# Kernel optimization log

Hardware: AMD Instinct MI355X
Metric: run time of the kernel (lower is better)

## Reference

```python
import jax, jax.numpy as jnp
import numpy as np

HIDDEN = 1024
HEADS = 16
HEAD_DIM = HIDDEN // HEADS


def setup_inputs() -> dict:
    key = jax.random.key(0)
    ks = jax.random.split(key, 5)
    x = jax.random.normal(ks[0], (4, 2048, HIDDEN), dtype=jnp.float32)
    s = 1.0 / np.sqrt(HIDDEN)
    W_qkv = jax.random.normal(ks[1], (HIDDEN, 3 * HIDDEN), dtype=jnp.float32) * s
    b_qkv = jax.random.normal(ks[2], (3 * HIDDEN,), dtype=jnp.float32) * s
    W_out = jax.random.normal(ks[3], (HIDDEN, HIDDEN), dtype=jnp.float32) * s
    b_out = jax.random.normal(ks[4], (HIDDEN,), dtype=jnp.float32) * s
    return {"x": x, "W_qkv": W_qkv, "b_qkv": b_qkv, "W_out": W_out, "b_out": b_out}


def reference(x, W_qkv, b_qkv, W_out, b_out):
    B, S, _ = x.shape
    qkv = x @ W_qkv + b_qkv                       # [B,S,3H]
    qkv = qkv.reshape(B, S, 3, HEADS, HEAD_DIM)
    q, k, v = jnp.moveaxis(qkv, 2, 0)             # each [B,S,nh,hd]
    scale = 1.0 / np.sqrt(HEAD_DIM)
    scores = jnp.einsum('bqhd,bkhd->bhqk', q, k) * scale
    probs = jax.nn.softmax(scores, axis=-1)       # dropout p=0 (eval): identity
    attn = jnp.einsum('bhqk,bkhd->bqhd', probs, v)
    attn = attn.reshape(B, S, HIDDEN)
    return attn @ W_out + b_out
```

## Files before the change

### kernel.cpp

```cpp
#include <hip/hip_runtime.h>

#define SEQ    2048
#define BATCH  4
#define HID    1024
#define NH     16
#define MTOT   (BATCH * SEQ)

typedef __attribute__((ext_vector_type(8)))  short          short8;
typedef __attribute__((ext_vector_type(4)))  float          f32x4;
typedef __attribute__((ext_vector_type(16))) float          f32x16;
typedef __attribute__((ext_vector_type(8)))  unsigned short ushort8v;

#define QSCL 0.1803368801111204f

__device__ __forceinline__ float bf2f(unsigned short u) {
    return __uint_as_float(((unsigned int)u) << 16);
}
__device__ __forceinline__ unsigned short f2bf(float f) {
    unsigned int u = __float_as_uint(f);
    u += 0x7fffu + ((u >> 16) & 1u);
    return (unsigned short)(u >> 16);
}
__device__ __forceinline__ unsigned int pk2bf(float lo, float hi) {
    unsigned int ul = __float_as_uint(lo) + 0x8000u;
    unsigned int uh = __float_as_uint(hi) + 0x8000u;
    return __builtin_amdgcn_perm(uh, ul, 0x07060302u);
}

__device__ __forceinline__ void gl_lds16(const void* g, void* l) {
    __builtin_amdgcn_global_load_lds(
        (__attribute__((address_space(1))) void*)g,
        (__attribute__((address_space(3))) void*)l, 16, 0, 0);
}

__device__ __forceinline__ int swz64(int row, int col) {
    return row * 64 + ((((col >> 3) ^ (row & 7))) << 3) + (col & 7);
}

__device__ __forceinline__ int gidx_of(int row, int kq) {
    return (row * 4 + ((kq + (row >> 1)) & 3)) * 8;
}

__global__ __launch_bounds__(256)
void cvt_x(const float* __restrict__ x, unsigned short* __restrict__ xb)
{
    const size_t i = ((size_t)blockIdx.x * 256 + threadIdx.x) * 4;
    const float4 f = *(const float4*)(x + i);
    uint2 u;
    u.x = pk2bf(f.x, f.y);
    u.y = pk2bf(f.z, f.w);
    *(uint2*)(xb + i) = u;
}

__global__ __launch_bounds__(256)
void transpose_cvt(const float* __restrict__ W, unsigned short* __restrict__ Wt,
                   int K, int N)
{
    __shared__ unsigned short T[32][33];
    const int n0 = blockIdx.x * 32, k0 = blockIdx.y * 32;
    const int tr = threadIdx.x >> 3, tc = (threadIdx.x & 7) * 4;
    const float4 f = *(const float4*)(W + (size_t)(k0 + tr) * N + n0 + tc);
    T[tr][tc + 0] = f2bf(f.x);
    T[tr][tc + 1] = f2bf(f.y);
    T[tr][tc + 2] = f2bf(f.z);
    T[tr][tc + 3] = f2bf(f.w);
    __syncthreads();
    ushort4 u;
    u.x = T[tc + 0][tr]; u.y = T[tc + 1][tr];
    u.z = T[tc + 2][tr]; u.w = T[tc + 3][tr];
    *(ushort4*)(Wt + (size_t)(n0 + tr) * K + k0 + tc) = u;
}

template<bool OUTF32, bool VSPLIT>
__global__ __launch_bounds__(256)
void gemm_mfma(const unsigned short* __restrict__ A,
               const unsigned short* __restrict__ Bt,
               const float* __restrict__ bias, void* __restrict__ Cptr,
               unsigned short* __restrict__ Vt,
               int lda, int ldc, int K)
{
    __shared__ unsigned short As[128 * 32];
    __shared__ unsigned short Bs[128 * 32];

    const int tid = threadIdx.x;
    const int wave = tid >> 6, lane = tid & 63;
    const int quad = lane >> 4, lm = lane & 15;
    const int wm = wave & 1, wn = wave >> 1;
    const int m0 = blockIdx.y * 128, n0 = blockIdx.x * 128;

    const unsigned short* aSrc[2];
    const unsigned short* bSrc[2];
    unsigned short* aDst[2];
    unsigned short* bDst[2];
    #pragma unroll
    for (int j = 0; j < 2; ++j) {
        const int g = (wave * 2 + j) * 64 + lane;
        const int row = g >> 2;
        const int kq = ((g & 3) - (row >> 1)) & 3;
        aSrc[j] = A  + (size_t)(m0 + row) * lda + kq * 8;
        bSrc[j] = Bt + (size_t)(n0 + row) * K   + kq * 8;
        aDst[j] = &As[g * 8];
        bDst[j] = &Bs[g * 8];
    }

    f32x4 acc[4][4];
    #pragma unroll
    for (int i = 0; i < 4; ++i)
        #pragma unroll
        for (int j = 0; j < 4; ++j)
            acc[i][j] = (f32x4){0.f, 0.f, 0.f, 0.f};

    int aOff[4], bOff[4];
    #pragma unroll
    for (int i = 0; i < 4; ++i) {
        aOff[i] = gidx_of(wm * 64 + i * 16 + lm, quad);
        bOff[i] = gidx_of(wn * 64 + i * 16 + lm, quad);
    }

    for (int k0 = 0; k0 < K; k0 += 32) {
        __syncthreads();
        gl_lds16(aSrc[0] + k0, aDst[0]);
        gl_lds16(aSrc[1] + k0, aDst[1]);
        gl_lds16(bSrc[0] + k0, bDst[0]);
        gl_lds16(bSrc[1] + k0, bDst[1]);
        __syncthreads();

        short8 af[4], bf[4];
        #pragma unroll
        for (int i = 0; i < 4; ++i) af[i] = *(const short8*)&As[aOff[i]];
        #pragma unroll
        for (int j = 0; j < 4; ++j) bf[j] = *(const short8*)&Bs[bOff[j]];
        #pragma unroll
        for (int i = 0; i < 4; ++i)
            #pragma unroll
            for (int j = 0; j < 4; ++j)
                acc[i][j] = __builtin_amdgcn_mfma_f32_16x16x32_bf16(
                    af[i], bf[j], acc[i][j], 0, 0, 0);
    }

    float bj[4];
    #pragma unroll
    for (int j = 0; j < 4; ++j) bj[j] = bias[n0 + wn * 64 + j * 16 + lm];

    #pragma unroll
    for (int i = 0; i < 4; ++i) {
        #pragma unroll
        for (int j = 0; j < 4; ++j) {
            const int col = n0 + wn * 64 + j * 16 + lm;
            #pragma unroll
            for (int rr = 0; rr < 4; ++rr) {
                const int row = m0 + wm * 64 + i * 16 + quad * 4 + rr;
                float v = acc[i][j][rr] + bj[j];
                if (VSPLIT) {
                    if (col >= 2048) {
                        const int dg = col - 2048;
                        const int b = row >> 11, s = row & 2047;
                        Vt[((size_t)b * 1024 + dg) * 2048 + s] = f2bf(v);
                    } else {
                        if (col < 1024) v *= QSCL;
                        ((unsigned short*)Cptr)[(size_t)row * ldc + col] = f2bf(v);
                    }
                } else if (OUTF32) {
                    ((float*)Cptr)[(size_t)row * ldc + col] = v;
                } else {
                    ((unsigned short*)Cptr)[(size_t)row * ldc + col] = f2bf(v);
                }
            }
        }
    }
}

__global__ __launch_bounds__(256, 2)
void attn_mfma(unsigned short* __restrict__ qk,
               const unsigned short* __restrict__ Vt)
{
    const int qt = blockIdx.x, hh = blockIdx.y, b = blockIdx.z;
    const size_t row0 = (size_t)b * SEQ;
    const int tid = threadIdx.x;
    const int wave = tid >> 6, lane = tid & 63;
    const int l5 = lane >> 5, lm = lane & 31;

    __shared__ unsigned short Ks[64 * 64];
    __shared__ unsigned short Vst[64 * 64];
    __shared__ unsigned short Ps[4][64 * 64];

    const int qbase = qt * 256 + wave * 64;

    short8 qf[2][4];
    #pragma unroll
    for (int qg = 0; qg < 2; ++qg)
        #pragma unroll
        for (int ks = 0; ks < 4; ++ks)
            qf[qg][ks] = *(const short8*)(
                qk + (row0 + qbase + qg * 32 + lm) * 2048 + hh * 64 + ks * 16 + l5 * 8);

    f32x16 oacc[2][2];
    #pragma unroll
    for (int dg = 0; dg < 2; ++dg)
        #pragma unroll
        for (int qg = 0; qg < 2; ++qg)
            #pragma unroll
            for (int e = 0; e < 16; ++e) oacc[dg][qg][e] = 0.f;
    float lrun[2] = {0.f, 0.f};

    const int srow = tid >> 2;
    const int scol = (tid & 3) * 16;

    const unsigned short* kbase = qk + 1024 + hh * 64;
    const unsigned short* vbase = Vt + ((size_t)b * 1024 + hh * 64 + srow) * 2048;

    ushort8v kp0, kp1, vp0, vp1;
    {
        const unsigned short* kp = kbase + (row0 + srow) * 2048 + scol;
        kp0 = *(const ushort8v*)kp;  kp1 = *(const ushort8v*)(kp + 8);
        vp0 = *(const ushort8v*)(vbase + scol);
        vp1 = *(const ushort8v*)(vbase + scol + 8);
    }

    for (int kt = 0; kt < SEQ; kt += 64) {
        __syncthreads();
        *(ushort8v*)&Ks[swz64(srow, scol)]      = kp0;
        *(ushort8v*)&Ks[swz64(srow, scol + 8)]  = kp1;
        *(ushort8v*)&Vst[swz64(srow, scol)]     = vp0;
        *(ushort8v*)&Vst[swz64(srow, scol + 8)] = vp1;
        __syncthreads();

        {
            const int nk = (kt + 64 < SEQ) ? kt + 64 : kt;
            const unsigned short* kp = kbase + (row0 + nk + srow) * 2048 + scol;
            kp0 = *(const ushort8v*)kp;  kp1 = *(const ushort8v*)(kp + 8);
            vp0 = *(const ushort8v*)(vbase + nk + scol);
            vp1 = *(const ushort8v*)(vbase + nk + scol + 8);
        }

        #pragma unroll
        for (int kg = 0; kg < 2; ++kg) {
            f32x16 s[2];
            #pragma unroll
            for (int qg = 0; qg < 2; ++qg)
                #pragma unroll
                for (int e = 0; e < 16; ++e) s[qg][e] = 0.f;
            #pragma unroll
            for (int ks = 0; ks < 4; ++ks) {
                const short8 aK =
                    *(const short8*)&Ks[swz64(kg * 32 + lm, ks * 16 + l5 * 8)];
                #pragma unroll
                for (int qg = 0; qg < 2; ++qg)
                    s[qg] = __builtin_amdgcn_mfma_f32_32x32x16_bf16(
                        aK, qf[qg][ks], s[qg], 0, 0, 0);
            }
            #pragma unroll
            for (int qg = 0; qg < 2; ++qg) {
                float ls = 0.f;
                #pragma unroll
                for (int rg = 0; rg < 4; ++rg) {
                    const float p0 = exp2f(s[qg][rg * 4 + 0]);
                    const float p1 = exp2f(s[qg][rg * 4 + 1]);
                    const float p2 = exp2f(s[qg][rg * 4 + 2]);
                    const float p3 = exp2f(s[qg][rg * 4 + 3]);
                    ls += (p0 + p1) + (p2 + p3);
                    uint2 pk;
                    pk.x = pk2bf(p0, p1);
                    pk.y = pk2bf(p2, p3);
                    *(uint2*)&Ps[wave][swz64(qg * 32 + lm,
                                             kg * 32 + rg * 8 + l5 * 4)] = pk;
                }
                lrun[qg] += ls;
            }
        }

        #pragma unroll
        for (int ks = 0; ks < 4; ++ks) {
            const short8 aV0 = *(const short8*)&Vst[swz64(lm,      ks * 16 + l5 * 8)];
            const short8 aV1 = *(const short8*)&Vst[swz64(32 + lm, ks * 16 + l5 * 8)];
            #pragma unroll
            for (int qg = 0; qg < 2; ++qg) {
                const short8 bP =
                    *(const short8*)&Ps[wave][swz64(qg * 32 + lm, ks * 16 + l5 * 8)];
                oacc[0][qg] = __builtin_amdgcn_mfma_f32_32x32x16_bf16(
                    aV0, bP, oacc[0][qg], 0, 0, 0);
                oacc[1][qg] = __builtin_amdgcn_mfma_f32_32x32x16_bf16(
                    aV1, bP, oacc[1][qg], 0, 0, 0);
            }
        }
    }

    float linv[2];
    #pragma unroll
    for (int qg = 0; qg < 2; ++qg) {
        const float lt = lrun[qg] + __shfl_xor(lrun[qg], 32);
        linv[qg] = 1.f / lt;
    }

    #pragma unroll
    for (int dg = 0; dg < 2; ++dg)
        #pragma unroll
        for (int qg = 0; qg < 2; ++qg) {
            unsigned short* orow =
                qk + (row0 + qbase + qg * 32 + lm) * 2048 + hh * 64;
            #pragma unroll
            for (int rg = 0; rg < 4; ++rg) {
                const int d0 = dg * 32 + rg * 8 + l5 * 4;
                ushort4 st;
                st.x = f2bf(oacc[dg][qg][rg * 4 + 0] * linv[qg]);
                st.y = f2bf(oacc[dg][qg][rg * 4 + 1] * linv[qg]);
                st.z = f2bf(oacc[dg][qg][rg * 4 + 2] * linv[qg]);
                st.w = f2bf(oacc[dg][qg][rg * 4 + 3] * linv[qg]);
                *(ushort4*)(orow + d0) = st;
            }
        }
}

__global__ __launch_bounds__(256)
void qproj(const float* __restrict__ A, const float* __restrict__ W,
           const float* __restrict__ bias, unsigned short* __restrict__ outus)
{
    __shared__ float As[64][17];
    __shared__ float Bs[16][64];
    const int tid = threadIdx.x;
    const int tx = tid & 15, ty = tid >> 4;
    const int m0 = blockIdx.y * 64, n0 = blockIdx.x * 64;
    const int ar = tid >> 2, ac = (tid & 3) * 4;
    const int br = tid >> 4, bc = (tid & 15) * 4;
    float acc[4][4] = {{0.f}};
    for (int k0 = 0; k0 < HID; k0 += 16) {
        const float4 av = *(const float4*)(A + (size_t)(m0 + ar) * HID + k0 + ac);
        As[ar][ac + 0] = av.x; As[ar][ac + 1] = av.y;
        As[ar][ac + 2] = av.z; As[ar][ac + 3] = av.w;
        *(float4*)&Bs[br][bc] =
            *(const float4*)(W + (size_t)(k0 + br) * 3072 + n0 + bc);
        __syncthreads();
        #pragma unroll
        for (int kk = 0; kk < 16; ++kk) {
            float a[4];
            #pragma unroll
            for (int i = 0; i < 4; ++i) a[i] = As[ty * 4 + i][kk];
            const float4 b4 = *(const float4*)&Bs[kk][tx * 4];
            const float bv[4] = {b4.x, b4.y, b4.z, b4.w};
            #pragma unroll
            for (int i = 0; i < 4; ++i)
                #pragma unroll
                for (int j = 0; j < 4; ++j)
                    acc[i][j] = fmaf(a[i], bv[j], acc[i][j]);
        }
        __syncthreads();
    }
    float bb[4];
    #pragma unroll
    for (int j = 0; j < 4; ++j) bb[j] = bias[n0 + tx * 4 + j];
    #pragma unroll
    for (int i = 0; i < 4; ++i) {
        ushort4 st;
        st.x = f2bf(acc[i][0] + bb[0]); st.y = f2bf(acc[i][1] + bb[1]);
        st.z = f2bf(acc[i][2] + bb[2]); st.w = f2bf(acc[i][3] + bb[3]);
        *(ushort4*)(outus + (size_t)(m0 + ty * 4 + i) * 2048 + 1024 + n0 + tx * 4) = st;
    }
}

__global__ __launch_bounds__(256)
void kv_inplace(const float* __restrict__ W, const float* __restrict__ bias,
                unsigned short* __restrict__ xu)
{
    const float* xf = (const float*)xu;
    __shared__ unsigned short Asb[16][1032];
    __shared__ float Bs[16][68];
    const int tid = threadIdx.x;
    const int m0 = blockIdx.x * 16;
    const int tx = tid & 15, ty = tid >> 4;
    #pragma unroll 4
    for (int i = 0; i < 16; ++i) {
        const float4 v = *(const float4*)(xf + (size_t)(m0 + i) * HID + tid * 4);
        ushort4 s;
        s.x = f2bf(v.x); s.y = f2bf(v.y); s.z = f2bf(v.z); s.w = f2bf(v.w);
        *(ushort4*)&Asb[i][tid * 4] = s;
    }
    __syncthreads();
    for (int n0 = 0; n0 < 2048; n0 += 64) {
        float acc[4] = {0.f, 0.f, 0.f, 0.f};
        for (int k0 = 0; k0 < HID; k0 += 16) {
            *(float4*)&Bs[ty][tx * 4] =
                *(const float4*)(W + (size_t)(k0 + ty) * 3072 + 1024 + n0 + tx * 4);
            __syncthreads();
            #pragma unroll
            for (int kk = 0; kk < 16; ++kk) {
                const float a = bf2f(Asb[ty][k0 + kk]);
                const float4 b4 = *(const float4*)&Bs[kk][tx * 4];
                acc[0] = fmaf(a, b4.x, acc[0]); acc[1] = fmaf(a, b4.y, acc[1]);
                acc[2] = fmaf(a, b4.z, acc[2]); acc[3] = fmaf(a, b4.w, acc[3]);
            }
            __syncthreads();
        }
        const int n = n0 + tx * 4;
        ushort4 s;
        s.x = f2bf(acc[0] + bias[1024 + n + 0]);
        s.y = f2bf(acc[1] + bias[1024 + n + 1]);
        s.z = f2bf(acc[2] + bias[1024 + n + 2]);
        s.w = f2bf(acc[3] + bias[1024 + n + 3]);
        *(ushort4*)(xu + (size_t)(m0 + ty) * 2048 + n) = s;
    }
}

__global__ __launch_bounds__(256)
void attn_fwd(const unsigned short* __restrict__ xu,
              unsigned short* __restrict__ outus)
{
    const int qt = blockIdx.x, h = blockIdx.y, b = blockIdx.z;
    const int s0 = qt * 16;
    const size_t row0 = (size_t)b * SEQ;
    const int tid = threadIdx.x;
    const int qi = tid >> 4, tj = tid & 15;
    __shared__ float Ksh[64][68];
    __shared__ float Vsh[64][68];
    __shared__ float Psh[16][68];
    float qreg[64];
    {
        const uint4* qp =
            (const uint4*)(outus + (row0 + s0 + qi) * 2048 + 1024 + h * 64);
        #pragma unroll
        for (int i = 0; i < 8; ++i) {
            uint4 u = qp[i];
            const unsigned int w[4] = {u.x, u.y, u.z, u.w};
            #pragma unroll
            for (int j = 0; j < 4; ++j) {
                qreg[i * 8 + j * 2 + 0] = __uint_as_float(w[j] << 16) * 0.125f;
                qreg[i * 8 + j * 2 + 1] = __uint_as_float(w[j] & 0xffff0000u) * 0.125f;
            }
        }
    }
    float mrun = -1e30f, lrunv = 0.f;
    float oacc[4] = {0.f, 0.f, 0.f, 0.f};
    const int lr = tid >> 3, lc = (tid & 7) * 8;
    for (int kt = 0; kt < SEQ; kt += 64) {
        __syncthreads();
        #pragma unroll
        for (int half = 0; half < 2; ++half) {
            const int r = lr + half * 32;
            const size_t rowoff = (row0 + kt + r) * 2048 + h * 64 + lc;
            uint4 ku = *(const uint4*)(xu + rowoff);
            uint4 vu = *(const uint4*)(xu + rowoff + 1024);
            float4 f0, f1;
            f0.x = __uint_as_float(ku.x << 16); f0.y = __uint_as_float(ku.x & 0xffff0000u);
            f0.z = __uint_as_float(ku.y << 16); f0.w = __uint_as_float(ku.y & 0xffff0000u);
            f1.x = __uint_as_float(ku.z << 16); f1.y = __uint_as_float(ku.z & 0xffff0000u);
            f1.z = __uint_as_float(ku.w << 16); f1.w = __uint_as_float(ku.w & 0xffff0000u);
            *(float4*)&Ksh[r][lc]     = f0;
            *(float4*)&Ksh[r][lc + 4] = f1;
            f0.x = __uint_as_float(vu.x << 16); f0.y = __uint_as_float(vu.x & 0xffff0000u);
            f0.z = __uint_as_float(vu.y << 16); f0.w = __uint_as_float(vu.y & 0xffff0000u);
            f1.x = __uint_as_float(vu.z << 16); f1.y = __uint_as_float(vu.z & 0xffff0000u);
            f1.z = __uint_as_float(vu.w << 16); f1.w = __uint_as_float(vu.w & 0xffff0000u);
            *(float4*)&Vsh[r][lc]     = f0;
            *(float4*)&Vsh[r][lc + 4] = f1;
        }
        __syncthreads();
        float sc[4];
        #pragma unroll
        for (int u = 0; u < 4; ++u) {
            const int kk = tj + 16 * u;
            float s = 0.f;
            #pragma unroll
            for (int d = 0; d < 64; ++d) s = fmaf(qreg[d], Ksh[kk][d], s);
            sc[u] = s;
        }
        float tmax = fmaxf(fmaxf(sc[0], sc[1]), fmaxf(sc[2], sc[3]));
        #pragma unroll
        for (int off = 8; off >= 1; off >>= 1)
            tmax = fmaxf(tmax, __shfl_xor(tmax, off, 16));
        const float mnew = fmaxf(mrun, tmax);
        const float alpha = __expf(mrun - mnew);
        float psum = 0.f;
        #pragma unroll
        for (int u = 0; u < 4; ++u) {
            const float p = __expf(sc[u] - mnew);
            Psh[qi][tj + 16 * u] = p;
            psum += p;
        }
        #pragma unroll
        for (int off = 8; off >= 1; off >>= 1)
            psum += __shfl_xor(psum, off, 16);
        lrunv = lrunv * alpha + psum;
        mrun = mnew;
        oacc[0] *= alpha; oacc[1] *= alpha; oacc[2] *= alpha; oacc[3] *= alpha;
        __syncthreads();
        #pragma unroll 8
        for (int kk = 0; kk < 64; ++kk) {
            const float p = Psh[qi][kk];
            const float4 v4 = *(const float4*)&Vsh[kk][tj * 4];
            oacc[0] = fmaf(p, v4.x, oacc[0]); oacc[1] = fmaf(p, v4.y, oacc[1]);
            oacc[2] = fmaf(p, v4.z, oacc[2]); oacc[3] = fmaf(p, v4.w, oacc[3]);
        }
    }
    const float inv = 1.f / lrunv;
    ushort4 st;
    st.x = f2bf(oacc[0] * inv); st.y = f2bf(oacc[1] * inv);
    st.z = f2bf(oacc[2] * inv); st.w = f2bf(oacc[3] * inv);
    *(ushort4*)(outus + (row0 + s0 + qi) * 2048 + h * 64 + tj * 4) = st;
}

__global__ __launch_bounds__(256)
void out_final(const float* __restrict__ W, const float* __restrict__ bias,
               unsigned short* __restrict__ outus)
{
    float* outf = (float*)outus;
    __shared__ unsigned short Asb[16][1032];
    __shared__ float Bs[16][68];
    const int tid = threadIdx.x;
    const int m0 = blockIdx.x * 16;
    const int tx = tid & 15, ty = tid >> 4;
    #pragma unroll 4
    for (int i = 0; i < 16; ++i)
        *(ushort4*)&Asb[i][tid * 4] =
            *(const ushort4*)(outus + (size_t)(m0 + i) * 2048 + tid * 4);
    __syncthreads();
    for (int n0 = 0; n0 < 1024; n0 += 64) {
        float acc[4] = {0.f, 0.f, 0.f, 0.f};
        for (int k0 = 0; k0 < HID; k0 += 16) {
            *(float4*)&Bs[ty][tx * 4] =
                *(const float4*)(W + (size_t)(k0 + ty) * HID + n0 + tx * 4);
            __syncthreads();
            #pragma unroll
            for (int kk = 0; kk < 16; ++kk) {
                const float a = bf2f(Asb[ty][k0 + kk]);
                const float4 b4 = *(const float4*)&Bs[kk][tx * 4];
                acc[0] = fmaf(a, b4.x, acc[0]); acc[1] = fmaf(a, b4.y, acc[1]);
                acc[2] = fmaf(a, b4.z, acc[2]); acc[3] = fmaf(a, b4.w, acc[3]);
            }
            __syncthreads();
        }
        const int n = n0 + tx * 4;
        float4 st;
        st.x = acc[0] + bias[n + 0]; st.y = acc[1] + bias[n + 1];
        st.z = acc[2] + bias[n + 2]; st.w = acc[3] + bias[n + 3];
        *(float4*)(outf + (size_t)(m0 + ty) * HID + n) = st;
    }
}

extern "C" void kernel_launch(void* const* d_in, const int* in_sizes, int n_in,
                              void* d_out, int out_size, void* d_ws, size_t ws_size,
                              hipStream_t stream) {
    const float* x     = (const float*)d_in[0];
    const float* W_qkv = (const float*)d_in[1];
    const float* b_qkv = (const float*)d_in[2];
    const float* W_out = (const float*)d_in[3];
    const float* b_out = (const float*)d_in[4];

    dim3 blk(256);

    if (ws_size >= (size_t)56 * 1024 * 1024) {
        unsigned short* qkbuf  = (unsigned short*)d_ws;
        unsigned short* vtbuf  = qkbuf + (size_t)MTOT * 2048;
        unsigned short* wqkv_t = vtbuf + (size_t)BATCH * NH * 64 * 2048;
        unsigned short* wout_t = wqkv_t + (size_t)3072 * 1024;
        unsigned short* xb     = (unsigned short*)d_out;

        cvt_x<<<dim3(MTOT * HID / 1024), blk, 0, stream>>>(x, xb);
        transpose_cvt<<<dim3(3072 / 32, 1024 / 32), blk, 0, stream>>>(
            W_qkv, wqkv_t, 1024, 3072);
        transpose_cvt<<<dim3(1024 / 32, 1024 / 32), blk, 0, stream>>>(
            W_out, wout_t, 1024, 1024);
        gemm_mfma<false, true><<<dim3(3072 / 128, MTOT / 128), blk, 0, stream>>>(
            xb, wqkv_t, b_qkv, (void*)qkbuf, vtbuf, 1024, 2048, 1024);
        attn_mfma<<<dim3(SEQ / 256, NH, BATCH), blk, 0, stream>>>(qkbuf, vtbuf);
        gemm_mfma<true, false><<<dim3(1024 / 128, MTOT / 128), blk, 0, stream>>>(
            qkbuf, wout_t, b_out, d_out, nullptr, 2048, 1024, 1024);
    } else {
        unsigned short* outus = (unsigned short*)d_out;
        unsigned short* xu    = (unsigned short*)d_in[0];
        qproj<<<dim3(HID / 64, MTOT / 64), blk, 0, stream>>>(x, W_qkv, b_qkv, outus);
        kv_inplace<<<dim3(MTOT / 16), blk, 0, stream>>>(W_qkv, b_qkv, xu);
        attn_fwd<<<dim3(SEQ / 16, NH, BATCH), blk, 0, stream>>>(xu, outus);
        out_final<<<dim3(MTOT / 16), blk, 0, stream>>>(W_out, b_out, outus);
    }
}
```

Before: 330.9 us.

## Double GEMM K-tile to 64 and switch attention exp from exp2 to natural exp

```diff
diff --git a/kernel.cpp b/kernel.cpp
--- a/kernel.cpp
+++ b/kernel.cpp
@@ -11,7 +11,7 @@
 typedef __attribute__((ext_vector_type(16))) float          f32x16;
 typedef __attribute__((ext_vector_type(8)))  unsigned short ushort8v;
 
-#define QSCL 0.1803368801111204f
+#define QSCL 0.125f
 
 __device__ __forceinline__ float bf2f(unsigned short u) {
     return __uint_as_float(((unsigned int)u) << 16);
@@ -37,8 +37,8 @@
     return row * 64 + ((((col >> 3) ^ (row & 7))) << 3) + (col & 7);
 }
 
-__device__ __forceinline__ int gidx_of(int row, int kq) {
-    return (row * 4 + ((kq + (row >> 1)) & 3)) * 8;
+__device__ __forceinline__ int gidx64(int row, int kq) {
+    return (row * 8 + ((kq + (row & 7)) & 7)) * 8;
 }
 
 __global__ __launch_bounds__(256)
@@ -79,8 +79,8 @@
                unsigned short* __restrict__ Vt,
                int lda, int ldc, int K)
 {
-    __shared__ unsigned short As[128 * 32];
-    __shared__ unsigned short Bs[128 * 32];
+    __shared__ unsigned short As[128 * 64];
+    __shared__ unsigned short Bs[128 * 64];
 
     const int tid = threadIdx.x;
     const int wave = tid >> 6, lane = tid & 63;
@@ -88,15 +88,15 @@
     const int wm = wave & 1, wn = wave >> 1;
     const int m0 = blockIdx.y * 128, n0 = blockIdx.x * 128;
 
-    const unsigned short* aSrc[2];
-    const unsigned short* bSrc[2];
-    unsigned short* aDst[2];
-    unsigned short* bDst[2];
-    #pragma unroll
-    for (int j = 0; j < 2; ++j) {
-        const int g = (wave * 2 + j) * 64 + lane;
-        const int row = g >> 2;
-        const int kq = ((g & 3) - (row >> 1)) & 3;
+    const unsigned short* aSrc[4];
+    const unsigned short* bSrc[4];
+    unsigned short* aDst[4];
+    unsigned short* bDst[4];
+    #pragma unroll
+    for (int j = 0; j < 4; ++j) {
+        const int g = (wave * 4 + j) * 64 + lane;
+        const int row = g >> 3;
+        const int kq = ((g & 7) - (row & 7)) & 7;
         aSrc[j] = A  + (size_t)(m0 + row) * lda + kq * 8;
         bSrc[j] = Bt + (size_t)(n0 + row) * K   + kq * 8;
         aDst[j] = &As[g * 8];
@@ -110,32 +110,37 @@
         for (int j = 0; j < 4; ++j)
             acc[i][j] = (f32x4){0.f, 0.f, 0.f, 0.f};
 
-    int aOff[4], bOff[4];
-    #pragma unroll
-    for (int i = 0; i < 4; ++i) {
-        aOff[i] = gidx_of(wm * 64 + i * 16 + lm, quad);
-        bOff[i] = gidx_of(wn * 64 + i * 16 + lm, quad);
-    }
-
-    for (int k0 = 0; k0 < K; k0 += 32) {
-        __syncthreads();
-        gl_lds16(aSrc[0] + k0, aDst[0]);
-        gl_lds16(aSrc[1] + k0, aDst[1]);
-        gl_lds16(bSrc[0] + k0, bDst[0]);
-        gl_lds16(bSrc[1] + k0, bDst[1]);
-        __syncthreads();
-
-        short8 af[4], bf[4];
-        #pragma unroll
-        for (int i = 0; i < 4; ++i) af[i] = *(const short8*)&As[aOff[i]];
-        #pragma unroll
-        for (int j = 0; j < 4; ++j) bf[j] = *(const short8*)&Bs[bOff[j]];
-        #pragma unroll
-        for (int i = 0; i < 4; ++i)
-            #pragma unroll
-            for (int j = 0; j < 4; ++j)
-                acc[i][j] = __builtin_amdgcn_mfma_f32_16x16x32_bf16(
-                    af[i], bf[j], acc[i][j], 0, 0, 0);
+    int aOff[2][4], bOff[2][4];
+    #pragma unroll
+    for (int h = 0; h < 2; ++h)
+        #pragma unroll
+        for (int i = 0; i < 4; ++i) {
+            aOff[h][i] = gidx64(wm * 64 + i * 16 + lm, h * 4 + quad);
+            bOff[h][i] = gidx64(wn * 64 + i * 16 + lm, h * 4 + quad);
+        }
+
+    for (int k0 = 0; k0 < K; k0 += 64) {
+        __syncthreads();
+        #pragma unroll
+        for (int j = 0; j < 4; ++j) gl_lds16(aSrc[j] + k0, aDst[j]);
+        #pragma unroll
+        for (int j = 0; j < 4; ++j) gl_lds16(bSrc[j] + k0, bDst[j]);
+        __syncthreads();
+
+        #pragma unroll
+        for (int h = 0; h < 2; ++h) {
+            short8 af[4], bf[4];
+            #pragma unroll
+            for (int i = 0; i < 4; ++i) af[i] = *(const short8*)&As[aOff[h][i]];
+            #pragma unroll
+            for (int j = 0; j < 4; ++j) bf[j] = *(const short8*)&Bs[bOff[h][j]];
+            #pragma unroll
+            for (int i = 0; i < 4; ++i)
+                #pragma unroll
+                for (int j = 0; j < 4; ++j)
+                    acc[i][j] = __builtin_amdgcn_mfma_f32_16x16x32_bf16(
+                        af[i], bf[j], acc[i][j], 0, 0, 0);
+        }
     }
 
     float bj[4];
@@ -254,10 +259,10 @@
                 float ls = 0.f;
                 #pragma unroll
                 for (int rg = 0; rg < 4; ++rg) {
-                    const float p0 = exp2f(s[qg][rg * 4 + 0]);
-                    const float p1 = exp2f(s[qg][rg * 4 + 1]);
-                    const float p2 = exp2f(s[qg][rg * 4 + 2]);
-                    const float p3 = exp2f(s[qg][rg * 4 + 3]);
+                    const float p0 = __expf(s[qg][rg * 4 + 0]);
+                    const float p1 = __expf(s[qg][rg * 4 + 1]);
+                    const float p2 = __expf(s[qg][rg * 4 + 2]);
+                    const float p3 = __expf(s[qg][rg * 4 + 3]);
                     ls += (p0 + p1) + (p2 + p3);
                     uint2 pk;
                     pk.x = pk2bf(p0, p1);
```

Measured after the change: 306.6 us. -7.4%, faster.
